# Kernel tuning notes

Hardware: AMD Instinct MI355X
Metric: run time of the kernel (lower is better)

## Reference

```python
import jax, jax.numpy as jnp
import numpy as np

LN_EPS = 1e-5

def setup_inputs() -> dict:
    key = jax.random.key(0)
    ks = jax.random.split(key, 4)
    B, C, L, P = 16, 512, 8192, 128
    return {
        "x": jax.random.normal(ks[0], (B, C, L), dtype=jnp.float32),
        "conv_mask_w": jax.random.normal(ks[1], (C,), dtype=jnp.float32) * (1.0 / np.sqrt(C)),
        "conv_mask_b": jnp.zeros((1,), dtype=jnp.float32),
        "w1": jax.random.normal(ks[2], (P, C), dtype=jnp.float32) * (1.0 / np.sqrt(C)),
        "b1": jnp.zeros((P,), dtype=jnp.float32),
        "ln_w": jnp.ones((P,), dtype=jnp.float32),
        "ln_b": jnp.zeros((P,), dtype=jnp.float32),
        "w2": jax.random.normal(ks[3], (C, P), dtype=jnp.float32) * (1.0 / np.sqrt(P)),
        "b2": jnp.zeros((C,), dtype=jnp.float32),
    }

def reference(x, conv_mask_w, conv_mask_b, w1, b1, ln_w, ln_b, w2, b2):
    # x: [B, C, L]
    # --- spatial_pool (pooling_type='att') ---
    # conv_mask: 1x1 Conv1d C->1 => per-position score
    scores = jnp.einsum('bcl,c->bl', x, conv_mask_w) + conv_mask_b  # [B, L]
    attn = jax.nn.softmax(scores, axis=-1)                          # softmax over L
    context = jnp.einsum('bcl,bl->bc', x, attn)                     # [B, C]
    # --- channel_add_conv: 1x1 conv -> LayerNorm([P,1]) -> ReLU -> 1x1 conv ---
    t = jnp.einsum('pc,bc->bp', w1, context) + b1                   # [B, P]
    mu = jnp.mean(t, axis=-1, keepdims=True)
    var = jnp.mean(jnp.square(t - mu), axis=-1, keepdims=True)
    t = (t - mu) * jax.lax.rsqrt(var + LN_EPS) * ln_w + ln_b
    t = jax.nn.relu(t)
    add_term = jnp.einsum('cp,bp->bc', w2, t) + b2                  # [B, C]
    return x + add_term[:, :, None]
```

## Files before the change

kernel.cpp:

```cpp
#include <hip/hip_runtime.h>
#include <math.h>

#define B 16
#define C 512
#define L 8192
#define PP 128
#define TILE_L 32
#define TPB 8
#define NB (L / (TILE_L * TPB))
#define LN_EPS 1e-5f

typedef float fx4 __attribute__((ext_vector_type(4)));

__global__ __launch_bounds__(512) void k_fused(
    const float* __restrict__ x, const float* __restrict__ cw,
    float* __restrict__ part_pc, float* __restrict__ part_m, float* __restrict__ part_z) {
  const int b = blockIdx.y;
  const int blk = blockIdx.x;
  const int tid = threadIdx.x;
  const int l_ofs = tid & 31;
  const int rg = tid >> 5;

  __shared__ float scw[C];
  __shared__ float sred[16][32];
  __shared__ float pw[TILE_L];
  __shared__ float s_m, s_z, s_resc;

  scw[tid] = cw[tid];
  if (tid == 0) { s_m = -INFINITY; s_z = 0.f; }

  float pc_acc = 0.f;
  const size_t xbase = (size_t)b * C * L;

  for (int t = 0; t < TPB; ++t) {
    const int l0 = (blk * TPB + t) * TILE_L;
    __syncthreads();

    float ps = 0.f;
    const float* xp = x + xbase + l0 + l_ofs;
    #pragma unroll
    for (int i = 0; i < 32; ++i) {
      const int c = (rg << 5) + i;
      ps += xp[(size_t)c * L] * scw[c];
    }
    sred[rg][l_ofs] = ps;
    __syncthreads();

    if (tid < 32) {
      float s = 0.f;
      #pragma unroll
      for (int g = 0; g < 16; ++g) s += sred[g][tid];
      float m = s;
      #pragma unroll
      for (int off = 16; off; off >>= 1) m = fmaxf(m, __shfl_xor(m, off, 32));
      const float mold = s_m;
      const float mnew = fmaxf(mold, m);
      const float p = __expf(s - mnew);
      float z = p;
      #pragma unroll
      for (int off = 16; off; off >>= 1) z += __shfl_xor(z, off, 32);
      pw[tid] = p;
      if (tid == 0) {
        const float resc = __expf(mold - mnew);
        s_resc = resc;
        s_z = s_z * resc + z;
        s_m = mnew;
      }
    }
    __syncthreads();

    const fx4* xr4 = (const fx4*)(x + xbase + (size_t)tid * L + l0);
    float pv = 0.f;
    #pragma unroll
    for (int j = 0; j < 8; ++j) {
      const fx4 v = xr4[j];
      pv += v.x * pw[4 * j] + v.y * pw[4 * j + 1] + v.z * pw[4 * j + 2] + v.w * pw[4 * j + 3];
    }
    pc_acc = pc_acc * s_resc + pv;
  }

  part_pc[(size_t)(b * NB + blk) * C + tid] = pc_acc;
  if (tid == 0) {
    part_m[b * NB + blk] = s_m;
    part_z[b * NB + blk] = s_z;
  }
}

__global__ void k_tail(const float* __restrict__ part_pc, const float* __restrict__ part_m,
                       const float* __restrict__ part_z,
                       const float* __restrict__ w1, const float* __restrict__ b1,
                       const float* __restrict__ lnw, const float* __restrict__ lnb,
                       const float* __restrict__ w2, const float* __restrict__ b2,
                       float* __restrict__ add_term) {
  const int b = blockIdx.x;
  const int tid = threadIdx.x;
  __shared__ float se[NB];
  __shared__ float sctx[C];
  __shared__ float st[PP];

  if (tid < 64) {
    const float m = (tid < NB) ? part_m[b * NB + tid] : -INFINITY;
    float M = m;
    #pragma unroll
    for (int off = 16; off; off >>= 1) M = fmaxf(M, __shfl_xor(M, off, 32));
    const float e = (tid < NB) ? __expf(m - M) : 0.f;
    float Z = (tid < NB) ? part_z[b * NB + tid] * e : 0.f;
    #pragma unroll
    for (int off = 16; off; off >>= 1) Z += __shfl_xor(Z, off, 32);
    if (tid < NB) se[tid] = e / Z;
  }
  __syncthreads();

  float acc = 0.f;
  const float* pp = part_pc + (size_t)b * NB * C + tid;
  #pragma unroll
  for (int t = 0; t < NB; ++t) acc += pp[(size_t)t * C] * se[t];
  sctx[tid] = acc;
  __syncthreads();

  {
    const int p = tid >> 2;
    const int q = tid & 3;
    const float* w1r = w1 + (size_t)p * C + q * 128;
    const float* cx = &sctx[q * 128];
    float a = 0.f;
    #pragma unroll 8
    for (int cc = 0; cc < 128; ++cc) a += w1r[cc] * cx[cc];
    a += __shfl_xor(a, 1);
    a += __shfl_xor(a, 2);
    if (q == 0) st[p] = a + b1[p];
  }
  __syncthreads();

  float tv = 0.f;
  if (tid < PP) {
    float mu = 0.f;
    #pragma unroll 8
    for (int pi = 0; pi < PP; ++pi) mu += st[pi];
    mu *= (1.f / PP);
    float var = 0.f;
    #pragma unroll 8
    for (int pi = 0; pi < PP; ++pi) { const float d = st[pi] - mu; var += d * d; }
    var *= (1.f / PP);
    tv = (st[tid] - mu) * rsqrtf(var + LN_EPS) * lnw[tid] + lnb[tid];
    tv = fmaxf(tv, 0.f);
  }
  __syncthreads();
  if (tid < PP) st[tid] = tv;
  __syncthreads();

  float a2 = b2[tid];
  const float* w2r = w2 + (size_t)tid * PP;
  #pragma unroll 8
  for (int pi = 0; pi < PP; ++pi) a2 += w2r[pi] * st[pi];
  add_term[b * C + tid] = a2;
}

__global__ void k_add(const float* __restrict__ x, const float* __restrict__ at,
                      float* __restrict__ out) {
  const int bc = blockIdx.x;
  const float a = at[bc];
  const fx4* xr = (const fx4*)(x + (size_t)bc * L);
  fx4* orow = (fx4*)(out + (size_t)bc * L);
  #pragma unroll 4
  for (int i = threadIdx.x; i < L / 4; i += 256) {
    fx4 v = xr[i];
    v = v + a;
    __builtin_nontemporal_store(v, &orow[i]);
  }
}

extern "C" void kernel_launch(void* const* d_in, const int* in_sizes, int n_in,
                              void* d_out, int out_size, void* d_ws, size_t ws_size,
                              hipStream_t stream) {
  const float* x   = (const float*)d_in[0];
  const float* cw  = (const float*)d_in[1];
  const float* w1  = (const float*)d_in[3];
  const float* b1  = (const float*)d_in[4];
  const float* lnw = (const float*)d_in[5];
  const float* lnb = (const float*)d_in[6];
  const float* w2  = (const float*)d_in[7];
  const float* b2  = (const float*)d_in[8];
  float* out = (float*)d_out;

  char* ws = (char*)d_ws;
  float* part_pc  = (float*)ws;
  float* part_m   = (float*)(ws + (size_t)B * NB * C * 4);
  float* part_z   = part_m + B * NB;
  float* add_term = part_z + B * NB;

  k_fused<<<dim3(NB, B), 512, 0, stream>>>(x, cw, part_pc, part_m, part_z);
  k_tail<<<dim3(B), C, 0, stream>>>(part_pc, part_m, part_z,
                                    w1, b1, lnw, lnb, w2, b2, add_term);
  k_add<<<dim3(B * C), 256, 0, stream>>>(x, add_term, out);
}
```

Baseline: 180.2 us.

## Hold x tiles in registers across score and context passes with double-buffered prefetch

The fused pooling kernel now loads each x tile once into registers as float4 vectors and reuses them for both the attention-score dot product and the weighted context accumulation. Before, each tile was read twice from global memory. It also prefetches the next tile while the current one is reduced, and moves to 1024-thread blocks with 64-wide tiles and wave shuffles for the reductions. The cost is heavier register use (16 float4 buffers plus 8 accumulators per thread) at 1024 threads, which may limit occupancy or cause spills. The number of partial blocks is unchanged, so the tail kernel stays compatible.

```diff
diff --git a/kernel.cpp b/kernel.cpp
--- a/kernel.cpp
+++ b/kernel.cpp
@@ -5,81 +5,115 @@
 #define C 512
 #define L 8192
 #define PP 128
-#define TILE_L 32
-#define TPB 8
-#define NB (L / (TILE_L * TPB))
+#define TL 64
+#define TPB 4
+#define NB (L / (TL * TPB))
 #define LN_EPS 1e-5f
 
 typedef float fx4 __attribute__((ext_vector_type(4)));
 
-__global__ __launch_bounds__(512) void k_fused(
+__global__ __launch_bounds__(1024) void k_fused(
     const float* __restrict__ x, const float* __restrict__ cw,
     float* __restrict__ part_pc, float* __restrict__ part_m, float* __restrict__ part_z) {
   const int b = blockIdx.y;
   const int blk = blockIdx.x;
   const int tid = threadIdx.x;
-  const int l_ofs = tid & 31;
-  const int rg = tid >> 5;
+  const int q = tid & 15;
+  const int r = tid >> 4;
+  const int lane = tid & 63;
+  const int w = tid >> 6;
 
   __shared__ float scw[C];
-  __shared__ float sred[16][32];
-  __shared__ float pw[TILE_L];
+  __shared__ float sred[16][TL] __attribute__((aligned(16)));
+  __shared__ float pw[TL] __attribute__((aligned(16)));
   __shared__ float s_m, s_z, s_resc;
 
-  scw[tid] = cw[tid];
+  if (tid < C) scw[tid] = cw[tid];
   if (tid == 0) { s_m = -INFINITY; s_z = 0.f; }
-
-  float pc_acc = 0.f;
-  const size_t xbase = (size_t)b * C * L;
-
-  for (int t = 0; t < TPB; ++t) {
-    const int l0 = (blk * TPB + t) * TILE_L;
+  __syncthreads();
+
+  float pc[8] = {0.f, 0.f, 0.f, 0.f, 0.f, 0.f, 0.f, 0.f};
+  const fx4* x4 = (const fx4*)(x + (size_t)b * C * L);
+  const int col0 = blk * TPB * (TL / 4) + q;
+
+  fx4 bufA[8], bufB[8];
+
+  #pragma unroll
+  for (int i = 0; i < 8; ++i)
+    bufA[i] = x4[(size_t)(r + 64 * i) * (L / 4) + col0];
+
+  auto tile_step = [&](fx4* xv, fx4* xn, int t) {
+    float sp0 = 0.f, sp1 = 0.f, sp2 = 0.f, sp3 = 0.f;
+    #pragma unroll
+    for (int i = 0; i < 8; ++i) {
+      const float wc = scw[r + 64 * i];
+      sp0 += xv[i].x * wc; sp1 += xv[i].y * wc;
+      sp2 += xv[i].z * wc; sp3 += xv[i].w * wc;
+    }
+    #pragma unroll
+    for (int m = 16; m <= 32; m <<= 1) {
+      sp0 += __shfl_xor(sp0, m); sp1 += __shfl_xor(sp1, m);
+      sp2 += __shfl_xor(sp2, m); sp3 += __shfl_xor(sp3, m);
+    }
+    if (lane < 16) {
+      fx4 v; v.x = sp0; v.y = sp1; v.z = sp2; v.w = sp3;
+      ((fx4*)&sred[w][0])[lane] = v;
+    }
+    if (t + 1 < TPB) {
+      const int col = col0 + (t + 1) * (TL / 4);
+      #pragma unroll
+      for (int i = 0; i < 8; ++i)
+        xn[i] = x4[(size_t)(r + 64 * i) * (L / 4) + col];
+    }
     __syncthreads();
 
-    float ps = 0.f;
-    const float* xp = x + xbase + l0 + l_ofs;
-    #pragma unroll
-    for (int i = 0; i < 32; ++i) {
-      const int c = (rg << 5) + i;
-      ps += xp[(size_t)c * L] * scw[c];
-    }
-    sred[rg][l_ofs] = ps;
-    __syncthreads();
-
-    if (tid < 32) {
+    if (tid < 64) {
       float s = 0.f;
       #pragma unroll
       for (int g = 0; g < 16; ++g) s += sred[g][tid];
       float m = s;
       #pragma unroll
-      for (int off = 16; off; off >>= 1) m = fmaxf(m, __shfl_xor(m, off, 32));
+      for (int off = 32; off; off >>= 1) m = fmaxf(m, __shfl_xor(m, off));
       const float mold = s_m;
       const float mnew = fmaxf(mold, m);
       const float p = __expf(s - mnew);
       float z = p;
       #pragma unroll
-      for (int off = 16; off; off >>= 1) z += __shfl_xor(z, off, 32);
+      for (int off = 32; off; off >>= 1) z += __shfl_xor(z, off);
       pw[tid] = p;
       if (tid == 0) {
-        const float resc = __expf(mold - mnew);
-        s_resc = resc;
-        s_z = s_z * resc + z;
+        const float e = __expf(mold - mnew);
+        s_resc = e;
+        s_z = s_z * e + z;
         s_m = mnew;
       }
     }
     __syncthreads();
 
-    const fx4* xr4 = (const fx4*)(x + xbase + (size_t)tid * L + l0);
-    float pv = 0.f;
-    #pragma unroll
-    for (int j = 0; j < 8; ++j) {
-      const fx4 v = xr4[j];
-      pv += v.x * pw[4 * j] + v.y * pw[4 * j + 1] + v.z * pw[4 * j + 2] + v.w * pw[4 * j + 3];
-    }
-    pc_acc = pc_acc * s_resc + pv;
-  }
-
-  part_pc[(size_t)(b * NB + blk) * C + tid] = pc_acc;
+    const float resc = s_resc;
+    const fx4 w4 = ((const fx4*)pw)[q];
+    #pragma unroll
+    for (int i = 0; i < 8; ++i) {
+      const float pv = xv[i].x * w4.x + xv[i].y * w4.y + xv[i].z * w4.z + xv[i].w * w4.w;
+      pc[i] = pc[i] * resc + pv;
+    }
+  };
+
+  tile_step(bufA, bufB, 0);
+  tile_step(bufB, bufA, 1);
+  tile_step(bufA, bufB, 2);
+  tile_step(bufB, bufA, 3);
+
+  #pragma unroll
+  for (int m = 1; m <= 8; m <<= 1) {
+    #pragma unroll
+    for (int i = 0; i < 8; ++i) pc[i] += __shfl_xor(pc[i], m);
+  }
+  if (q == 0) {
+    float* dst = part_pc + (size_t)(b * NB + blk) * C;
+    #pragma unroll
+    for (int i = 0; i < 8; ++i) dst[r + 64 * i] = pc[i];
+  }
   if (tid == 0) {
     part_m[b * NB + blk] = s_m;
     part_z[b * NB + blk] = s_z;
@@ -120,15 +154,15 @@
 
   {
     const int p = tid >> 2;
-    const int q = tid & 3;
-    const float* w1r = w1 + (size_t)p * C + q * 128;
-    const float* cx = &sctx[q * 128];
+    const int qq = tid & 3;
+    const float* w1r = w1 + (size_t)p * C + qq * 128;
+    const float* cx = &sctx[qq * 128];
     float a = 0.f;
     #pragma unroll 8
     for (int cc = 0; cc < 128; ++cc) a += w1r[cc] * cx[cc];
     a += __shfl_xor(a, 1);
     a += __shfl_xor(a, 2);
-    if (q == 0) st[p] = a + b1[p];
+    if (qq == 0) st[p] = a + b1[p];
   }
   __syncthreads();
 
@@ -189,7 +223,7 @@
   float* part_z   = part_m + B * NB;
   float* add_term = part_z + B * NB;
 
-  k_fused<<<dim3(NB, B), 512, 0, stream>>>(x, cw, part_pc, part_m, part_z);
+  k_fused<<<dim3(NB, B), 1024, 0, stream>>>(x, cw, part_pc, part_m, part_z);
   k_tail<<<dim3(B), C, 0, stream>>>(part_pc, part_m, part_z,
                                     w1, b1, lnw, lnb, w2, b2, add_term);
   k_add<<<dim3(B * C), 256, 0, stream>>>(x, add_term, out);
```

Result: slower. 193.1 us (+7.1%).
